# Kernel optimization log

Measured on AMD Instinct MI355X. Metric: run time of the kernel, lower is better.

The kernel has to match this reference:

```python
import jax, jax.numpy as jnp
import numpy as np

B, N, C = 4, 2048, 1024
H = 8
D = C // H  # head dim = 128
SCALE = D ** -0.5
EPS = 1e-5


def setup_inputs() -> dict:
    key = jax.random.key(0)
    ks = jax.random.split(key, 12)
    s = 0.02
    return {
        "x": jax.random.normal(ks[0], (B, N, C), jnp.float32),
        "ln1_g": jnp.ones((C,), jnp.float32),
        "ln1_b": jnp.zeros((C,), jnp.float32),
        "w_qkv": jax.random.normal(ks[1], (3 * C, C), jnp.float32) * s,  # torch Linear weight [out,in], no bias
        "w_proj": jax.random.normal(ks[2], (C, C), jnp.float32) * s,
        "b_proj": jnp.zeros((C,), jnp.float32),
        "ln2_g": jnp.ones((C,), jnp.float32),
        "ln2_b": jnp.zeros((C,), jnp.float32),
        "w1": jax.random.normal(ks[3], (C, C), jnp.float32) * s,
        "b1": jnp.full((C,), 0.1, jnp.float32),
        "w2": jax.random.normal(ks[4], (C, C), jnp.float32) * s,
        "b2": jnp.full((C,), 0.1, jnp.float32),
        "bn_g": jnp.ones((C,), jnp.float32),
        "bn_b": jnp.zeros((C,), jnp.float32),
        "bn_mean": jnp.zeros((C,), jnp.float32),
        "bn_var": jnp.ones((C,), jnp.float32),
    }


def _layernorm(x, g, b):
    mu = jnp.mean(x, axis=-1, keepdims=True)
    var = jnp.mean(jnp.square(x - mu), axis=-1, keepdims=True)
    return (x - mu) * jax.lax.rsqrt(var + EPS) * g + b


def reference(x, ln1_g, ln1_b, w_qkv, w_proj, b_proj, ln2_g, ln2_b,
              w1, b1, w2, b2, bn_g, bn_b, bn_mean, bn_var):
    # --- attention branch (pre-LN) ---
    h = _layernorm(x, ln1_g, ln1_b)
    qkv = h @ w_qkv.T                              # [B,N,3C]
    qkv = qkv.reshape(B, N, 3, H, D)
    q = qkv[:, :, 0].transpose(0, 2, 1, 3)         # [B,H,N,D]
    k = qkv[:, :, 1].transpose(0, 2, 1, 3)
    v = qkv[:, :, 2].transpose(0, 2, 1, 3)
    attn = jnp.einsum('bhnd,bhmd->bhnm', q, k) * SCALE
    attn = jax.nn.softmax(attn, axis=-1)
    o = jnp.einsum('bhnm,bhmd->bhnd', attn, v)     # [B,H,N,D]
    o = o.transpose(0, 2, 1, 3).reshape(B, N, C)
    x = x + (o @ w_proj.T + b_proj)

    # --- MLP branch (pre-LN), ELU + eval-mode BatchNorm ---
    h = _layernorm(x, ln2_g, ln2_b)
    h = jax.nn.elu(h @ w1.T + b1)
    h = jax.nn.elu(h @ w2.T + b2)
    h = (h - bn_mean) * jax.lax.rsqrt(bn_var + EPS) * bn_g + bn_b
    return x + h
```

## Files before the change

kernel.cpp:

```cpp
#include <hip/hip_runtime.h>
#include <hip/hip_bf16.h>

using u16 = unsigned short;
typedef __attribute__((ext_vector_type(8))) __bf16 bf16x8;
typedef __attribute__((ext_vector_type(4))) float f32x4;
typedef __attribute__((ext_vector_type(16))) float f32x16;
typedef __attribute__((ext_vector_type(4))) unsigned int u32x4;
typedef __attribute__((ext_vector_type(2))) unsigned int u32x2;

#define LN_EPS 1e-5f
#define ATT_SCALE 0.08838834764831845f

__device__ __forceinline__ u16 f2bf(float f) {
    unsigned int u = __builtin_bit_cast(unsigned int, f);
    u += 0x7FFFu + ((u >> 16) & 1u);
    return (u16)(u >> 16);
}

__device__ __forceinline__ bf16x8 ld_frag(const u16* p) {
    return __builtin_bit_cast(bf16x8, *(const u32x4*)p);
}

__device__ __forceinline__ unsigned pack_bf2(float lo, float hi) {
    return __builtin_amdgcn_perm(__builtin_bit_cast(unsigned, hi),
                                 __builtin_bit_cast(unsigned, lo), 0x07060302u);
}

__device__ __forceinline__ void gl_lds(const u16* g, u16* l) {
    __builtin_amdgcn_global_load_lds((const __attribute__((address_space(1))) void*)g,
                                     (__attribute__((address_space(3))) void*)l, 16, 0, 0);
}

__global__ __launch_bounds__(256)
void cvt_ln(const float* __restrict__ x, const float* __restrict__ g,
            const float* __restrict__ b, u16* __restrict__ hout,
            const float* __restrict__ w_qkv, const float* __restrict__ w_proj,
            const float* __restrict__ w1, const float* __restrict__ w2,
            u16* __restrict__ wout)
{
    const int t = threadIdx.x;
    if (blockIdx.x < 8192) {
        const int row = blockIdx.x;
        const float4 v = ((const float4*)(x + (size_t)row * 1024))[t];
        float s  = v.x + v.y + v.z + v.w;
        float ss = v.x * v.x + v.y * v.y + v.z * v.z + v.w * v.w;
        #pragma unroll
        for (int d = 32; d > 0; d >>= 1) { s += __shfl_down(s, d); ss += __shfl_down(ss, d); }
        __shared__ float red[8];
        const int wave = t >> 6, lane = t & 63;
        if (lane == 0) { red[wave] = s; red[4 + wave] = ss; }
        __syncthreads();
        const float S  = red[0] + red[1] + red[2] + red[3];
        const float SS = red[4] + red[5] + red[6] + red[7];
        const float mu = S * (1.f / 1024.f);
        const float rstd = rsqrtf(SS * (1.f / 1024.f) - mu * mu + LN_EPS);
        const float4 gv = ((const float4*)g)[t];
        const float4 bv = ((const float4*)b)[t];
        ushort4 ov;
        ov.x = f2bf((v.x - mu) * rstd * gv.x + bv.x);
        ov.y = f2bf((v.y - mu) * rstd * gv.y + bv.y);
        ov.z = f2bf((v.z - mu) * rstd * gv.z + bv.z);
        ov.w = f2bf((v.w - mu) * rstd * gv.w + bv.w);
        ((ushort4*)(hout + (size_t)row * 1024))[t] = ov;
    } else {
        const int i = (blockIdx.x - 8192) * 256 + t;
        const int n_qkv = 3072 * 1024 / 4, n_c = 1024 * 1024 / 4;
        const float* src;
        int j = i;
        if (j < n_qkv) { src = w_qkv; }
        else if ((j -= n_qkv) < n_c) { src = w_proj; }
        else if ((j -= n_c) < n_c)   { src = w1; }
        else { j -= n_c; src = w2; }
        const float4 v = ((const float4*)src)[j];
        ushort4 o;
        o.x = f2bf(v.x); o.y = f2bf(v.y); o.z = f2bf(v.z); o.w = f2bf(v.w);
        ((ushort4*)wout)[i] = o;
    }
}

__global__ __launch_bounds__(256)
void ln_kernel(const float* __restrict__ x, const float* __restrict__ g,
               const float* __restrict__ b, u16* __restrict__ out)
{
    const int row = blockIdx.x;
    const int t = threadIdx.x;
    const float4 v = ((const float4*)(x + (size_t)row * 1024))[t];
    float s  = v.x + v.y + v.z + v.w;
    float ss = v.x * v.x + v.y * v.y + v.z * v.z + v.w * v.w;
    #pragma unroll
    for (int d = 32; d > 0; d >>= 1) { s += __shfl_down(s, d); ss += __shfl_down(ss, d); }
    __shared__ float red[8];
    const int wave = t >> 6, lane = t & 63;
    if (lane == 0) { red[wave] = s; red[4 + wave] = ss; }
    __syncthreads();
    const float S  = red[0] + red[1] + red[2] + red[3];
    const float SS = red[4] + red[5] + red[6] + red[7];
    const float mu = S * (1.f / 1024.f);
    const float rstd = rsqrtf(SS * (1.f / 1024.f) - mu * mu + LN_EPS);
    const float4 gv = ((const float4*)g)[t];
    const float4 bv = ((const float4*)b)[t];
    ushort4 ov;
    ov.x = f2bf((v.x - mu) * rstd * gv.x + bv.x);
    ov.y = f2bf((v.y - mu) * rstd * gv.y + bv.y);
    ov.z = f2bf((v.z - mu) * rstd * gv.z + bv.z);
    ov.w = f2bf((v.w - mu) * rstd * gv.w + bv.w);
    ((ushort4*)(out + (size_t)row * 1024))[t] = ov;
}


#define GEMM_PREAMBLE(Aptr, Bptr, Kdim)                                           \
    __shared__ __align__(16) u16 As[128 * 64];                                    \
    __shared__ __align__(16) u16 Bs[128 * 64];                                    \
    const int tid  = threadIdx.x;                                                 \
    const int wave = tid >> 6;                                                    \
    const int lane = tid & 63;                                                    \
    const int quad = lane >> 4;                                                   \
    const int l16  = lane & 15;                                                   \
    const int m0 = blockIdx.x * 128;                                              \
    const int n0 = blockIdx.y * 128;                                              \
    const int wm = (wave & 1) * 64;                                               \
    const int wn = (wave >> 1) * 64;                                              \
    f32x4 acc[4][4];                                                              \
    _Pragma("unroll")                                                             \
    for (int i = 0; i < 4; i++)                                                   \
        _Pragma("unroll")                                                         \
        for (int j = 0; j < 4; j++)                                               \
            acc[i][j] = f32x4{0.f, 0.f, 0.f, 0.f};                                \
    const int srow8 = lane >> 3;                  \
    const int scol  = ((lane & 7) ^ srow8) * 8;    \
    const u16* gA = Aptr + (size_t)(m0 + wave * 8 + srow8) * Kdim + scol;         \
    const u16* gB = Bptr + (size_t)(n0 + wave * 8 + srow8) * Kdim + scol;         \
    u16* lA = &As[wave * 512];                                                    \
    u16* lB = &Bs[wave * 512];                                                    \
    for (int k0 = 0; k0 < Kdim; k0 += 64) {                                       \
        _Pragma("unroll")                                                         \
        for (int rnd = 0; rnd < 4; rnd++) {                                       \
            gl_lds(gA + (size_t)rnd * 32 * Kdim + k0, lA + rnd * 2048);           \
            gl_lds(gB + (size_t)rnd * 32 * Kdim + k0, lB + rnd * 2048);           \
        }                                                                         \
        __syncthreads();                                                          \
        _Pragma("unroll")                                                         \
        for (int kk = 0; kk < 2; kk++) {                                          \
            bf16x8 af[4], bfv[4];                                                 \
            _Pragma("unroll")                                                     \
            for (int i = 0; i < 4; i++) {                                         \
                const int row = wm + i * 16 + l16;                                \
                const int c = (kk * 4 + quad) ^ (row & 7);                        \
                af[i] = ld_frag(&As[row * 64 + c * 8]);                           \
            }                                                                     \
            _Pragma("unroll")                                                     \
            for (int j = 0; j < 4; j++) {                                         \
                const int row = wn + j * 16 + l16;                                \
                const int c = (kk * 4 + quad) ^ (row & 7);                        \
                bfv[j] = ld_frag(&Bs[row * 64 + c * 8]);                          \
            }                                                                     \
            _Pragma("unroll")                                                     \
            for (int i = 0; i < 4; i++)                                           \
                _Pragma("unroll")                                                 \
                for (int j = 0; j < 4; j++)                                       \
                    acc[i][j] = __builtin_amdgcn_mfma_f32_16x16x32_bf16(          \
                        af[i], bfv[j], acc[i][j], 0, 0, 0);                       \
        }                                                                         \
        __syncthreads();                                                          \
    }

__global__ __launch_bounds__(256, 3)
void gemm_qkv(const u16* __restrict__ A, const u16* __restrict__ Bw,
              u16* __restrict__ Cb, u16* __restrict__ Cv)
{
    GEMM_PREAMBLE(A, Bw, 1024)

    #pragma unroll
    for (int j = 0; j < 4; j++) {
        const int gn = n0 + wn + j * 16 + l16;
        if (gn < 2048) {
            const float qs = (gn < 1024) ? ATT_SCALE : 1.0f;
            #pragma unroll
            for (int i = 0; i < 4; i++) {
                const int gm0 = m0 + wm + i * 16 + quad * 4;
                #pragma unroll
                for (int r = 0; r < 4; r++)
                    Cb[(size_t)(gm0 + r) * 2048 + gn] = f2bf(acc[i][j][r] * qs);
            }
        } else {
            const int hh = (gn >> 7) & 7, dd = gn & 127;
            #pragma unroll
            for (int i = 0; i < 4; i++) {
                const int gm0 = m0 + wm + i * 16 + quad * 4;
                #pragma unroll
                for (int r = 0; r < 4; r++) {
                    const int tok = gm0 + r;
                    Cv[((size_t)((tok >> 11) * 8 + hh) * 128 + dd) * 2048 + (tok & 2047)] =
                        f2bf(acc[i][j][r]);
                }
            }
        }
    }
}

template <int EPI>
__global__ __launch_bounds__(256, 3)
void gemm_c(const u16* __restrict__ A, const u16* __restrict__ Bw,
            const float* __restrict__ bias, const float* __restrict__ res,
            float* __restrict__ Cf, u16* __restrict__ Cb,
            const float* __restrict__ bng, const float* __restrict__ bnb,
            const float* __restrict__ bnm, const float* __restrict__ bnv)
{
    const int N = 1024;
    GEMM_PREAMBLE(A, Bw, 1024)

    #pragma unroll
    for (int j = 0; j < 4; j++) {
        const int gn = n0 + wn + j * 16 + l16;
        float bs = bias[gn], sc = 0.f, sh = 0.f;
        if constexpr (EPI == 3) {
            const float iv = rsqrtf(bnv[gn] + LN_EPS);
            sc = bng[gn] * iv;
            sh = bnb[gn] - bnm[gn] * sc;
        }
        #pragma unroll
        for (int i = 0; i < 4; i++) {
            const int gm0 = m0 + wm + i * 16 + quad * 4;
            #pragma unroll
            for (int r = 0; r < 4; r++) {
                const size_t idx = (size_t)(gm0 + r) * N + gn;
                const float v = acc[i][j][r];
                if constexpr (EPI == 1) {
                    Cf[idx] = res[idx] + v + bs;
                } else if constexpr (EPI == 2) {
                    float t = v + bs;
                    t = t > 0.f ? t : (__expf(t) - 1.f);
                    Cb[idx] = f2bf(t);
                } else {
                    float t = v + bs;
                    t = t > 0.f ? t : (__expf(t) - 1.f);
                    t = t * sc + sh;
                    Cf[idx] = res[idx] + t;
                }
            }
        }
    }
}

__global__ __launch_bounds__(256, 2)
void attn_kernel(const u16* __restrict__ qk, const u16* __restrict__ vT, u16* __restrict__ o)
{
    __shared__ __align__(16) u16 smem[32768];

    const int tid  = threadIdx.x;
    const int wave = tid >> 6;
    const int lane = tid & 63;
    const int l32  = lane & 31;
    const int hl   = lane >> 5;
    const int id   = blockIdx.x;
    const int bh   = ((id >> 7) << 3) | (id & 7);
    const int qt   = (id >> 3) & 15;
    const int b    = bh >> 3, h = bh & 7;
    const size_t tok0 = (size_t)b * 2048;

    const u16* qptr = qk + h * 128;
    const u16* kptr = qk + 1024 + h * 128;
    const u16* vptr = vT + (size_t)bh * 128 * 2048;

    #pragma unroll
    for (int qq = 0; qq < 8; qq++) {
        const int s = qq * 256 + tid;
        const int r = s >> 4;
        const int cg = (s & 15) ^ (r & 7);
        const u16* g = qptr + (tok0 + qt * 128 + r) * 2048 + cg * 8;
        const int sb = 16384 + (qq * 256 + (tid & 192)) * 8;
        gl_lds(g, smem + sb);
    }
    __syncthreads();

    bf16x8 qf[8];
    {
        const int row = wave * 32 + l32;
        #pragma unroll
        for (int ks = 0; ks < 8; ks++) {
            const int c = (ks * 2 + hl) ^ (row & 7);
            qf[ks] = ld_frag(smem + 16384 + row * 128 + c * 8);
        }
    }

    f32x16 oacc[4];
    #pragma unroll
    for (int i = 0; i < 4; i++)
        #pragma unroll
        for (int e = 0; e < 16; e++) oacc[i][e] = 0.f;
    float l_acc = 0.f;

    {
        #pragma unroll
        for (int qq = 0; qq < 4; qq++) {
            const int s = qq * 256 + tid;
            const int rk = s >> 4, ck = (s & 15) ^ (rk & 7);
            gl_lds(kptr + (tok0 + rk) * 2048 + ck * 8,
                   smem + (qq * 256 + (tid & 192)) * 8);
            const int rv = s >> 3, cv = (s & 7) ^ (rv & 7);
            gl_lds(vptr + (size_t)rv * 2048 + cv * 8,
                   smem + 8192 + (qq * 256 + (tid & 192)) * 8);
        }
    }

    for (int kt = 0; kt < 32; kt++) {
        __syncthreads();

        if (kt + 1 < 32) {
            u16* nb = smem + ((kt + 1) & 1) * 16384;
            #pragma unroll
            for (int qq = 0; qq < 4; qq++) {
                const int s = qq * 256 + tid;
                const int rk = s >> 4, ck = (s & 15) ^ (rk & 7);
                gl_lds(kptr + (tok0 + (kt + 1) * 64 + rk) * 2048 + ck * 8,
                       nb + (qq * 256 + (tid & 192)) * 8);
                const int rv = s >> 3, cv = (s & 7) ^ (rv & 7);
                gl_lds(vptr + (size_t)rv * 2048 + (kt + 1) * 64 + cv * 8,
                       nb + 8192 + (qq * 256 + (tid & 192)) * 8);
            }
        }

        const u16* Ks = smem + (kt & 1) * 16384;
        const u16* Vs = Ks + 8192;

        f32x16 sacc[2];
        #pragma unroll
        for (int t = 0; t < 2; t++)
            #pragma unroll
            for (int e = 0; e < 16; e++) sacc[t][e] = 0.f;
        __builtin_amdgcn_s_setprio(1);
        #pragma unroll
        for (int ks = 0; ks < 8; ks++) {
            #pragma unroll
            for (int mt = 0; mt < 2; mt++) {
                const int row = mt * 32 + l32;
                const int c = (ks * 2 + hl) ^ (row & 7);
                const bf16x8 kf = ld_frag(Ks + row * 128 + c * 8);
                sacc[mt] = __builtin_amdgcn_mfma_f32_32x32x16_bf16(kf, qf[ks], sacc[mt], 0, 0, 0);
            }
        }
        __builtin_amdgcn_s_setprio(0);

        unsigned pk[2][8];
        #pragma unroll
        for (int t = 0; t < 2; t++) {
            #pragma unroll
            for (int r2 = 0; r2 < 8; r2++) {
                const float p0 = __expf(sacc[t][2 * r2]);
                const float p1 = __expf(sacc[t][2 * r2 + 1]);
                l_acc += p0 + p1;
                pk[t][r2] = pack_bf2(p0, p1);
            }
        }

        #pragma unroll
        for (int ks = 0; ks < 4; ks++) {
            const int t = ks >> 1;
            const int pb = (ks & 1) * 4;
            const u32x2 r02 = __builtin_amdgcn_permlane32_swap(pk[t][pb + 0], pk[t][pb + 2], false, false);
            const u32x2 r13 = __builtin_amdgcn_permlane32_swap(pk[t][pb + 1], pk[t][pb + 3], false, false);
            u32x4 pu;
            pu.x = r02.x; pu.y = r13.x; pu.z = r02.y; pu.w = r13.y;
            const bf16x8 pf = __builtin_bit_cast(bf16x8, pu);
            __builtin_amdgcn_s_setprio(1);
            #pragma unroll
            for (int dt = 0; dt < 4; dt++) {
                const int row = dt * 32 + l32;
                const int c = (ks * 2 + hl) ^ (row & 7);
                const bf16x8 vf = ld_frag(Vs + row * 64 + c * 8);
                oacc[dt] = __builtin_amdgcn_mfma_f32_32x32x16_bf16(vf, pf, oacc[dt], 0, 0, 0);
            }
            __builtin_amdgcn_s_setprio(0);
        }
    }

    __syncthreads();
    u16* Ot = smem;
    const float lt  = l_acc + __shfl_xor(l_acc, 32);
    const float inv = 1.0f / lt;
    const int qloc = wave * 32 + l32;
    #pragma unroll
    for (int dt = 0; dt < 4; dt++) {
        #pragma unroll
        for (int r2 = 0; r2 < 8; r2++) {
            const float v0 = oacc[dt][2 * r2] * inv;
            const float v1 = oacc[dt][2 * r2 + 1] * inv;
            const int dp = dt * 32 + 4 * hl + 2 * (r2 & 1) + 8 * (r2 >> 1);
            *(unsigned*)(Ot + qloc * 136 + dp) = pack_bf2(v0, v1);
        }
    }
    __syncthreads();
    const int qr = tid >> 1;
    const int hh = tid & 1;
    const u16* src = Ot + qr * 136 + hh * 64;
    u16* dst = o + (tok0 + qt * 128 + qr) * 1024 + h * 128 + hh * 64;
    #pragma unroll
    for (int c = 0; c < 8; c++)
        *(u32x4*)(dst + c * 8) = *(const u32x4*)(src + c * 8);
}

extern "C" void kernel_launch(void* const* d_in, const int* in_sizes, int n_in,
                              void* d_out, int out_size, void* d_ws, size_t ws_size,
                              hipStream_t stream)
{
    const float* x      = (const float*)d_in[0];
    const float* ln1_g  = (const float*)d_in[1];
    const float* ln1_b  = (const float*)d_in[2];
    const float* w_qkv  = (const float*)d_in[3];
    const float* w_proj = (const float*)d_in[4];
    const float* b_proj = (const float*)d_in[5];
    const float* ln2_g  = (const float*)d_in[6];
    const float* ln2_b  = (const float*)d_in[7];
    const float* w1     = (const float*)d_in[8];
    const float* b1     = (const float*)d_in[9];
    const float* w2     = (const float*)d_in[10];
    const float* b2     = (const float*)d_in[11];
    const float* bn_g   = (const float*)d_in[12];
    const float* bn_b   = (const float*)d_in[13];
    const float* bn_m   = (const float*)d_in[14];
    const float* bn_v   = (const float*)d_in[15];
    float* out = (float*)d_out;

    u16* wq   = (u16*)d_ws;
    u16* wp   = wq  + (size_t)3072 * 1024;
    u16* w1b  = wp  + (size_t)1024 * 1024;
    u16* w2b  = w1b + (size_t)1024 * 1024;
    u16* hbuf = w2b + (size_t)1024 * 1024;
    u16* qkb  = hbuf + (size_t)8192 * 1024;
    u16* vTb  = qkb + (size_t)8192 * 2048;
    u16* obuf = vTb + (size_t)8192 * 1024;
    float* x1 = (float*)(obuf + (size_t)8192 * 1024);

    cvt_ln<<<14336, 256, 0, stream>>>(x, ln1_g, ln1_b, hbuf, w_qkv, w_proj, w1, w2, wq);

    gemm_qkv<<<dim3(64, 24), 256, 0, stream>>>(hbuf, wq, qkb, vTb);

    attn_kernel<<<512, 256, 0, stream>>>(qkb, vTb, obuf);

    gemm_c<1><<<dim3(64, 8), 256, 0, stream>>>(obuf, wp,
        b_proj, x, x1, nullptr, nullptr, nullptr, nullptr, nullptr);

    ln_kernel<<<8192, 256, 0, stream>>>(x1, ln2_g, ln2_b, hbuf);

    gemm_c<2><<<dim3(64, 8), 256, 0, stream>>>(hbuf, w1b,
        b1, nullptr, nullptr, obuf, nullptr, nullptr, nullptr, nullptr);

    gemm_c<3><<<dim3(64, 8), 256, 0, stream>>>(obuf, w2b,
        b2, x1, out, nullptr, bn_g, bn_b, bn_m, bn_v);
}
```

Measured before the change: 361.8 us.

## Pipeline GEMM global-to-LDS loads with a four-stage ring buffer

Replaces the single-buffered 64-wide K tile in the shared GEMM mainloop with a four-buffer ring of 32-wide K tiles. Loads are issued three stages ahead, and explicit vmcnt waits plus barriers gate each stage. The LDS swizzle and staging layout change to match the 32-column tiles, MFMA sections get raised wave priority, and launch bounds drop from 3 to 2 blocks per SU. This is meant to hide global memory latency behind MFMA work, at the cost of lower occupancy and more barriers per K step.

```diff
diff --git a/kernel.cpp b/kernel.cpp
--- a/kernel.cpp
+++ b/kernel.cpp
@@ -107,10 +107,14 @@
     ((ushort4*)(out + (size_t)row * 1024))[t] = ov;
 }
 
+#define WAITVM12 { asm volatile("s_waitcnt vmcnt(12)" ::: "memory"); __builtin_amdgcn_sched_barrier(0); }
+#define WAITVM8  { asm volatile("s_waitcnt vmcnt(8)"  ::: "memory"); __builtin_amdgcn_sched_barrier(0); }
+#define WAITVM4  { asm volatile("s_waitcnt vmcnt(4)"  ::: "memory"); __builtin_amdgcn_sched_barrier(0); }
+#define WAITVM0  { asm volatile("s_waitcnt vmcnt(0)"  ::: "memory"); __builtin_amdgcn_sched_barrier(0); }
 
 #define GEMM_PREAMBLE(Aptr, Bptr, Kdim)                                           \
-    __shared__ __align__(16) u16 As[128 * 64];                                    \
-    __shared__ __align__(16) u16 Bs[128 * 64];                                    \
+    __shared__ __align__(16) u16 As[4][128 * 32];                                 \
+    __shared__ __align__(16) u16 Bs[4][128 * 32];                                 \
     const int tid  = threadIdx.x;                                                 \
     const int wave = tid >> 6;                                                    \
     const int lane = tid & 63;                                                    \
@@ -126,45 +130,60 @@
         _Pragma("unroll")                                                         \
         for (int j = 0; j < 4; j++)                                               \
             acc[i][j] = f32x4{0.f, 0.f, 0.f, 0.f};                                \
-    const int srow8 = lane >> 3;                  \
-    const int scol  = ((lane & 7) ^ srow8) * 8;    \
-    const u16* gA = Aptr + (size_t)(m0 + wave * 8 + srow8) * Kdim + scol;         \
-    const u16* gB = Bptr + (size_t)(n0 + wave * 8 + srow8) * Kdim + scol;         \
-    u16* lA = &As[wave * 512];                                                    \
-    u16* lB = &Bs[wave * 512];                                                    \
-    for (int k0 = 0; k0 < Kdim; k0 += 64) {                                       \
+    \
+    \
+    const u16* gA = Aptr + (size_t)(m0 + (tid >> 2)) * Kdim                       \
+                    + (((tid & 3) ^ ((tid >> 3) & 3)) * 8);                       \
+    const u16* gB = Bptr + (size_t)(n0 + (tid >> 2)) * Kdim                       \
+                    + (((tid & 3) ^ ((tid >> 3) & 3)) * 8);                       \
+    auto STAGE = [&](int kt, int bf) {                                            \
         _Pragma("unroll")                                                         \
-        for (int rnd = 0; rnd < 4; rnd++) {                                       \
-            gl_lds(gA + (size_t)rnd * 32 * Kdim + k0, lA + rnd * 2048);           \
-            gl_lds(gB + (size_t)rnd * 32 * Kdim + k0, lB + rnd * 2048);           \
+        for (int rnd = 0; rnd < 2; rnd++) {                                       \
+            gl_lds(gA + (size_t)rnd * 64 * Kdim + kt * 32,                        \
+                   &As[bf][rnd * 2048 + wave * 512]);                             \
+            gl_lds(gB + (size_t)rnd * 64 * Kdim + kt * 32,                        \
+                   &Bs[bf][rnd * 2048 + wave * 512]);                             \
         }                                                                         \
-        __syncthreads();                                                          \
+    };                                                                            \
+    const int NT = Kdim / 32;                                                     \
+    STAGE(0, 0); STAGE(1, 1); STAGE(2, 2);                                        \
+    for (int t = 0; t < NT; t++) {                                                \
+        __builtin_amdgcn_sched_barrier(0);                                        \
+        __builtin_amdgcn_s_barrier();         \
+        __builtin_amdgcn_sched_barrier(0);                                        \
+        if (t + 3 < NT) STAGE(t + 3, (t + 3) & 3);                                \
+        if (t < NT - 3)       WAITVM12                                            \
+        else if (t == NT - 3) WAITVM8                                             \
+        else if (t == NT - 2) WAITVM4                                             \
+        else                  WAITVM0                                             \
+        __builtin_amdgcn_s_barrier();        \
+        __builtin_amdgcn_sched_barrier(0);                                        \
+        const u16* curA = As[t & 3];                                              \
+        const u16* curB = Bs[t & 3];                                              \
+        bf16x8 af[4], bfv[4];                                                     \
         _Pragma("unroll")                                                         \
-        for (int kk = 0; kk < 2; kk++) {                                          \
-            bf16x8 af[4], bfv[4];                                                 \
+        for (int i = 0; i < 4; i++) {                                             \
+            const int row = wm + i * 16 + l16;                                    \
+            const int c = quad ^ ((row >> 1) & 3);                                \
+            af[i] = ld_frag(&curA[row * 32 + c * 8]);                             \
+        }                                                                         \
+        _Pragma("unroll")                                                         \
+        for (int j = 0; j < 4; j++) {                                             \
+            const int row = wn + j * 16 + l16;                                    \
+            const int c = quad ^ ((row >> 1) & 3);                                \
+            bfv[j] = ld_frag(&curB[row * 32 + c * 8]);                            \
+        }                                                                         \
+        __builtin_amdgcn_s_setprio(1);                                            \
+        _Pragma("unroll")                                                         \
+        for (int i = 0; i < 4; i++)                                               \
             _Pragma("unroll")                                                     \
-            for (int i = 0; i < 4; i++) {                                         \
-                const int row = wm + i * 16 + l16;                                \
-                const int c = (kk * 4 + quad) ^ (row & 7);                        \
-                af[i] = ld_frag(&As[row * 64 + c * 8]);                           \
-            }                                                                     \
-            _Pragma("unroll")                                                     \
-            for (int j = 0; j < 4; j++) {                                         \
-                const int row = wn + j * 16 + l16;                                \
-                const int c = (kk * 4 + quad) ^ (row & 7);                        \
-                bfv[j] = ld_frag(&Bs[row * 64 + c * 8]);                          \
-            }                                                                     \
-            _Pragma("unroll")                                                     \
-            for (int i = 0; i < 4; i++)                                           \
-                _Pragma("unroll")                                                 \
-                for (int j = 0; j < 4; j++)                                       \
-                    acc[i][j] = __builtin_amdgcn_mfma_f32_16x16x32_bf16(          \
-                        af[i], bfv[j], acc[i][j], 0, 0, 0);                       \
-        }                                                                         \
-        __syncthreads();                                                          \
-    }
-
-__global__ __launch_bounds__(256, 3)
+            for (int j = 0; j < 4; j++)                                           \
+                acc[i][j] = __builtin_amdgcn_mfma_f32_16x16x32_bf16(              \
+                    af[i], bfv[j], acc[i][j], 0, 0, 0);                           \
+        __builtin_amdgcn_s_setprio(0);                                            \
+    }
+
+__global__ __launch_bounds__(256, 2)
 void gemm_qkv(const u16* __restrict__ A, const u16* __restrict__ Bw,
               u16* __restrict__ Cb, u16* __restrict__ Cv)
 {
@@ -199,7 +218,7 @@
 }
 
 template <int EPI>
-__global__ __launch_bounds__(256, 3)
+__global__ __launch_bounds__(256, 2)
 void gemm_c(const u16* __restrict__ A, const u16* __restrict__ Bw,
             const float* __restrict__ bias, const float* __restrict__ res,
             float* __restrict__ Cf, u16* __restrict__ Cb,
```

Result: slower. 382.6 us (+5.7%).
